# Kernel optimization log

Hardware: AMD Instinct MI355X
Metric: run time of the kernel (lower is better)

The kernel has to match this reference:

```python
import jax, jax.numpy as jnp
import numpy as np

CLUSTER_DIM = 64
SHRINKAGE = True
EPS = 1e-8


def setup_inputs() -> dict:
    key = jax.random.key(0)
    x = jax.random.normal(key, (256, CLUSTER_DIM, 4096), dtype=jnp.float32)
    return {"x": x}


def _mat_shrinkage(C, n):
    # Rao-Blackwellized Ledoit-Wolf shrinkage toward scaled identity.
    p = CLUSTER_DIM
    I = jnp.eye(p, dtype=C.dtype)[None, :, :]
    trace = jnp.trace(C, axis1=-2, axis2=-1)[:, None, None]          # [B,1,1]
    F_hat = trace / p * I
    second_trace = jnp.einsum('bij,bji->b', C, C)[:, None, None]      # tr(C @ C)
    numerator = (n - 2) / n * second_trace + trace ** 2
    denominator = (n + 2) * (second_trace - trace ** 2 / p)
    rho = jnp.minimum(numerator / denominator, 1.0)
    return rho * F_hat + (1.0 - rho) * C


def reference(x):
    B, C, M = x.shape  # C == CLUSTER_DIM
    x_mu = jnp.mean(x, axis=2, keepdims=True)
    x_cnt = x - x_mu                                                  # [B,C,M]
    cov = jnp.einsum('bcm,bdm->bcd', x_cnt, x_cnt) / M                # [B,C,C]
    if SHRINKAGE:
        cov = _mat_shrinkage(cov, n=M)
    L, Q = jnp.linalg.eigh(cov)                                       # L:[B,C] Q:[B,C,C]
    L = jnp.maximum(L, EPS)
    # S_hat = Q @ diag(L^-1/2) @ Q^T, fused as scaled columns of Q
    S_hat = jnp.einsum('bik,bk,bjk->bij', Q, jax.lax.rsqrt(L), Q)     # [B,C,C]
    Z = jnp.einsum('bij,bjm->bim', S_hat, x_cnt)                      # [B,C,M]
    return Z
```

## Files before the change

kernel.cpp:

```cpp
#include <hip/hip_runtime.h>
#include <hip/hip_bf16.h>

#define BB 256
#define P 64
#define MM 4096
#define MC 128
#define MT 256

using bf16x8 = __attribute__((ext_vector_type(8))) short;
using f32x16 = __attribute__((ext_vector_type(16))) float;

__device__ inline unsigned bfh(float a) {
    unsigned u = __float_as_uint(a);
    return (u + 0x7fffu + ((u >> 16) & 1u)) >> 16;
}
__device__ inline f32x16 MF(bf16x8 a, bf16x8 b, f32x16 c) {
    return __builtin_amdgcn_mfma_f32_32x32x16_bf16(a, b, c, 0, 0, 0);
}

__global__ __launch_bounds__(256)
void covpart_kernel(const float* __restrict__ x, float* __restrict__ s2p,
                    float* __restrict__ s1p, int nsplit)
{
    __shared__ __align__(16) unsigned char smem[17408];
    char* xh = (char*)smem;

    const int b = blockIdx.x, sp = blockIdx.y;
    const int t = threadIdx.x;
    const int w = t >> 6, l = t & 63;
    const int lr = l & 31, lh = l >> 5;
    const int mlen = MM / nsplit;
    const float* xb = x + (size_t)b * (P * MM) + (size_t)sp * mlen;

    f32x16 acc0 = {0,0,0,0,0,0,0,0,0,0,0,0,0,0,0,0};
    f32x16 acc1 = {0,0,0,0,0,0,0,0,0,0,0,0,0,0,0,0};
    f32x16 acc2 = {0,0,0,0,0,0,0,0,0,0,0,0,0,0,0,0};
    float s1a[8] = {0.f,0.f,0.f,0.f,0.f,0.f,0.f,0.f};

    const int kbase = lh * 16;

    const int nch = mlen / MC;
    for (int ch = 0; ch < nch; ++ch) {
        const int m0 = ch * MC;
        __syncthreads();
        float4 v[8];
        #pragma unroll
        for (int j = 0; j < 8; ++j) {
            int f4 = t + 256 * j;
            int r = f4 >> 5, c = (f4 & 31) << 2;
            v[j] = *reinterpret_cast<const float4*>(xb + (size_t)r * MM + m0 + c);
        }
        #pragma unroll
        for (int j = 0; j < 8; ++j) {
            int f4 = t + 256 * j;
            int r = f4 >> 5, c4 = f4 & 31;
            float e0 = v[j].x, e1 = v[j].y, e2 = v[j].z, e3 = v[j].w;
            s1a[j] += (e0 + e1) + (e2 + e3);
            uint2 hp;
            hp.x = bfh(e0) | (bfh(e1) << 16);
            hp.y = bfh(e2) | (bfh(e3) << 16);
            *reinterpret_cast<uint2*>(xh + r * 272 + c4 * 8) = hp;
        }
        __syncthreads();
        #pragma unroll
        for (int kk = 0; kk < 2; ++kk) {
            const int kb = (2 * w + kk) * 32 + kbase;
            bf16x8 f0 = *(const bf16x8*)(xh + lr * 272 + kb);
            bf16x8 f1 = *(const bf16x8*)(xh + (32 + lr) * 272 + kb);
            acc0 = MF(f0, f0, acc0);
            acc1 = MF(f0, f1, acc1);
            acc2 = MF(f1, f1, acc2);
        }
    }

    float (*T)[32][33] = reinterpret_cast<float (*)[32][33]>(smem);
    float* s2b = s2p + ((size_t)sp * BB + b) * (P * P);

#define REDUCE_PASS(ACC, STORE)                                       \
    {                                                                 \
        __syncthreads();                                              \
        _Pragma("unroll")                                             \
        for (int n = 0; n < 16; ++n) {                                \
            int row = (n & 3) + 8 * (n >> 2) + 4 * lh;                \
            T[w][row][lr] = ACC[n];                                   \
        }                                                             \
        __syncthreads();                                              \
        _Pragma("unroll")                                             \
        for (int q = 0; q < 4; ++q) {                                 \
            int idx = t + 256 * q;                                    \
            int r = idx >> 5, c = idx & 31;                           \
            float s = T[0][r][c] + T[1][r][c] + T[2][r][c] + T[3][r][c]; \
            STORE                                                     \
        }                                                             \
    }

    REDUCE_PASS(acc0, s2b[r * 64 + c] = s;)
    REDUCE_PASS(acc1, s2b[r * 64 + 32 + c] = s; s2b[(32 + c) * 64 + r] = s;)
    REDUCE_PASS(acc2, s2b[(32 + r) * 64 + 32 + c] = s;)
#undef REDUCE_PASS

    #pragma unroll
    for (int m = 16; m >= 1; m >>= 1) {
        #pragma unroll
        for (int j = 0; j < 8; ++j) s1a[j] += __shfl_xor(s1a[j], m);
    }
    if ((l & 31) == 0) {
        float* s1b = s1p + ((size_t)sp * BB + b) * P;
        int r0 = 2 * w + lh;
        #pragma unroll
        for (int j = 0; j < 8; ++j) s1b[r0 + 8 * j] = s1a[j];
    }
}

typedef float (*Mat68)[68];

__device__ inline void mm64f(Mat68 D, Mat68 A, Mat68 Bm, int t, float alpha, float beta)
{
    __syncthreads();
    const int r0 = (t >> 4) * 4, c0 = (t & 15) * 4;
    float acc[4][4];
    #pragma unroll
    for (int i = 0; i < 4; ++i)
        #pragma unroll
        for (int j = 0; j < 4; ++j) acc[i][j] = 0.f;
    #pragma unroll 4
    for (int k = 0; k < P; ++k) {
        float av[4], bv[4];
        *reinterpret_cast<float4*>(av) = *reinterpret_cast<const float4*>(&A[k][r0]);
        *reinterpret_cast<float4*>(bv) = *reinterpret_cast<const float4*>(&Bm[k][c0]);
        #pragma unroll
        for (int i = 0; i < 4; ++i)
            #pragma unroll
            for (int j = 0; j < 4; ++j) acc[i][j] += av[i] * bv[j];
    }
    __syncthreads();
    #pragma unroll
    for (int i = 0; i < 4; ++i)
        #pragma unroll
        for (int j = 0; j < 4; ++j)
            D[r0 + i][c0 + j] = alpha * acc[i][j] + ((r0 + i) == (c0 + j) ? beta : 0.f);
}

__global__ __launch_bounds__(256)
void whiten_kernel(const float* __restrict__ s2p, const float* __restrict__ s1p,
                   float* __restrict__ shat, float* __restrict__ tvec, int nsplit)
{
    __shared__ __align__(16) float B0[P][68], B1[P][68], B2[P][68], B3[P][68], B4[P][68];
    __shared__ float mus[P];
    __shared__ float red[2][4];
    const int b = blockIdx.x, t = threadIdx.x;

    if (t < P) {
        float s = 0.f;
        for (int sp = 0; sp < nsplit; ++sp) s += s1p[((size_t)sp * BB + b) * P + t];
        mus[t] = s * (1.0f / MM);
    }
    __syncthreads();

    float tr_part = 0.f, s2_part = 0.f;
    #pragma unroll
    for (int j = 0; j < 16; ++j) {
        int f = t + 256 * j;
        int i = f >> 6, jc = f & 63;
        float sum = 0.f;
        for (int sp = 0; sp < nsplit; ++sp)
            sum += s2p[((size_t)sp * BB + b) * (P * P) + f];
        float v = sum * (1.0f / MM) - mus[i] * mus[jc];
        B0[i][jc] = v;
        s2_part += v * v;
        if (i == jc) tr_part += v;
    }
    #pragma unroll
    for (int off = 32; off > 0; off >>= 1) {
        tr_part += __shfl_down(tr_part, off);
        s2_part += __shfl_down(s2_part, off);
    }
    if ((t & 63) == 0) { red[0][t >> 6] = tr_part; red[1][t >> 6] = s2_part; }
    __syncthreads();
    const float trace = red[0][0] + red[0][1] + red[0][2] + red[0][3];
    const float sum2  = red[1][0] + red[1][1] + red[1][2] + red[1][3];

    const float nf = (float)MM;
    const float num = (nf - 2.0f) / nf * sum2 + trace * trace;
    const float den = (nf + 2.0f) * (sum2 - trace * trace / (float)P);
    const float rho = (den > 0.f) ? fminf(num / den, 1.0f) : 1.0f;
    const float lam = trace * (1.0f / P);
    const float inv_s = 1.0f / lam;

    #pragma unroll
    for (int j = 0; j < 16; ++j) {
        int f = t + 256 * j;
        int i = f >> 6, jc = f & 63;
        float v = B0[i][jc];
        float sv = ((1.0f - rho) * v + ((i == jc) ? rho * lam : 0.f)) * inv_s;
        B0[i][jc] = sv;
        B2[i][jc] = ((i == jc) ? 1.5f : 0.f) - 0.5f * sv;
    }

    mm64f(B1, B0, B2, t, 1.f, 0.f);
    Mat68 Yc = B1, Zc = B2, Tc = B0, U = B3, V = B4;
    {
        mm64f(Tc, Zc, Yc, t, -0.5f, 1.5f);
        mm64f(U,  Yc, Tc, t, 1.f, 0.f);
        mm64f(V,  Tc, Zc, t, 1.f, 0.f);
        Mat68 tmp = Yc; Yc = U; U = tmp;
        tmp = Zc; Zc = V; V = tmp;
    }
    mm64f(Tc, Zc, Yc, t, -0.5f, 1.5f);
    mm64f(U,  Tc, Zc, t, 1.f, 0.f);
    __syncthreads();

    const float sc = rsqrtf(lam);
    float* sb = shat + (size_t)b * (P * P);
    #pragma unroll
    for (int j = 0; j < 16; ++j) {
        int f = t + 256 * j;
        int i = f >> 6, jc = f & 63;
        sb[f] = U[i][jc] * sc;
    }
    if (t < P) {
        float tv = 0.f;
        #pragma unroll
        for (int d = 0; d < P; ++d) tv += U[t][d] * mus[d];
        tvec[b * P + t] = tv * sc;
    }
}

__global__ __launch_bounds__(256)
void apply_kernel(const float* __restrict__ x, const float* __restrict__ shat,
                  const float* __restrict__ tvec, float* __restrict__ out)
{
    __shared__ __align__(16) float Ss[P][P];
    __shared__ __align__(16) float Xs[P][MT];
    const int mt = blockIdx.x, b = blockIdx.y;
    const int t = threadIdx.x;
    const float* xb = x + (size_t)b * (P * MM) + mt * MT;
    const float* sb = shat + (size_t)b * (P * P);

    #pragma unroll
    for (int j = 0; j < 4; ++j) {
        int f4 = t + 256 * j;
        *reinterpret_cast<float4*>(&Ss[f4 >> 4][(f4 & 15) * 4]) =
            *reinterpret_cast<const float4*>(sb + (size_t)f4 * 4);
    }
    #pragma unroll
    for (int j = 0; j < 16; ++j) {
        int f4 = t + 256 * j;
        int r = f4 >> 6, c = (f4 & 63) * 4;
        *reinterpret_cast<float4*>(&Xs[r][c]) =
            *reinterpret_cast<const float4*>(xb + (size_t)r * MM + c);
    }
    __syncthreads();

    const int w = t >> 6, l = t & 63;
    const int r0 = (w & 1) * 32 + (l >> 4) * 8;
    const int c0 = (w >> 1) * 128 + (l & 15) * 4;
    float acc[8][8];
    #pragma unroll
    for (int i = 0; i < 8; ++i)
        #pragma unroll
        for (int j = 0; j < 8; ++j) acc[i][j] = 0.f;

    for (int d = 0; d < P; ++d) {
        float sv[8], xv[8];
        *reinterpret_cast<float4*>(&sv[0]) = *reinterpret_cast<const float4*>(&Ss[d][r0]);
        *reinterpret_cast<float4*>(&sv[4]) = *reinterpret_cast<const float4*>(&Ss[d][r0 + 4]);
        *reinterpret_cast<float4*>(&xv[0]) = *reinterpret_cast<const float4*>(&Xs[d][c0]);
        *reinterpret_cast<float4*>(&xv[4]) = *reinterpret_cast<const float4*>(&Xs[d][c0 + 64]);
        #pragma unroll
        for (int i = 0; i < 8; ++i)
            #pragma unroll
            for (int j = 0; j < 8; ++j)
                acc[i][j] += sv[i] * xv[j];
    }

    float tv[8];
    *reinterpret_cast<float4*>(&tv[0]) = *reinterpret_cast<const float4*>(tvec + b * P + r0);
    *reinterpret_cast<float4*>(&tv[4]) = *reinterpret_cast<const float4*>(tvec + b * P + r0 + 4);
    float* ob = out + (size_t)b * (P * MM) + mt * MT;
    #pragma unroll
    for (int i = 0; i < 8; ++i) {
        float4 v0 = make_float4(acc[i][0] - tv[i], acc[i][1] - tv[i],
                                acc[i][2] - tv[i], acc[i][3] - tv[i]);
        float4 v1 = make_float4(acc[i][4] - tv[i], acc[i][5] - tv[i],
                                acc[i][6] - tv[i], acc[i][7] - tv[i]);
        *reinterpret_cast<float4*>(ob + (size_t)(r0 + i) * MM + c0)      = v0;
        *reinterpret_cast<float4*>(ob + (size_t)(r0 + i) * MM + c0 + 64) = v1;
    }
}

extern "C" void kernel_launch(void* const* d_in, const int* in_sizes, int n_in,
                              void* d_out, int out_size, void* d_ws, size_t ws_size,
                              hipStream_t stream)
{
    const float* x = (const float*)d_in[0];
    float* out = (float*)d_out;

    auto need = [](int ns) -> size_t {
        return ((size_t)ns * BB * P * P + (size_t)ns * BB * P
                + (size_t)BB * P * P + (size_t)BB * P) * sizeof(float);
    };
    int nsplit = 4;
    if (ws_size < need(4)) nsplit = 2;
    if (ws_size < need(2)) nsplit = 1;

    float* s2p  = (float*)d_ws;
    float* s1p  = s2p + (size_t)nsplit * BB * P * P;
    float* shat = s1p + (size_t)nsplit * BB * P;
    float* tvec = shat + (size_t)BB * P * P;

    covpart_kernel<<<dim3(BB, nsplit), 256, 0, stream>>>(x, s2p, s1p, nsplit);
    whiten_kernel<<<dim3(BB), 256, 0, stream>>>(s2p, s1p, shat, tvec, nsplit);
    apply_kernel<<<dim3(MM / MT, BB), 256, 0, stream>>>(x, shat, tvec, out);
}
```

Measured before the change: 215.8 us.

## Use bf16 MFMA for the whitening apply GEMM and hardware bf16 pack

The apply kernel now stages the whitening matrix as bf16 and packs pairs of x rows into bf16 in shared memory, then computes the 64x256 output tile with 32x32x16 bf16 MFMA instead of an fp32 FMA outer-product loop. The whiten kernel writes the scaled whitening matrix directly as packed bf16. The software round-to-nearest bf16 conversion in the covariance kernel is replaced by the v_cvt_pk_bf16_f32 instruction. This removes most of the scalar FMA work in the apply stage at the cost of bf16 precision on the output GEMM and scalar, less coalesced output stores.

```diff
diff --git a/kernel.cpp b/kernel.cpp
--- a/kernel.cpp
+++ b/kernel.cpp
@@ -10,12 +10,13 @@
 using bf16x8 = __attribute__((ext_vector_type(8))) short;
 using f32x16 = __attribute__((ext_vector_type(16))) float;
 
-__device__ inline unsigned bfh(float a) {
-    unsigned u = __float_as_uint(a);
-    return (u + 0x7fffu + ((u >> 16) & 1u)) >> 16;
-}
 __device__ inline f32x16 MF(bf16x8 a, bf16x8 b, f32x16 c) {
     return __builtin_amdgcn_mfma_f32_32x32x16_bf16(a, b, c, 0, 0, 0);
+}
+__device__ inline unsigned cvtpk(float lo, float hi) {
+    unsigned u;
+    asm("v_cvt_pk_bf16_f32 %0, %1, %2" : "=v"(u) : "v"(lo), "v"(hi));
+    return u;
 }
 
 __global__ __launch_bounds__(256)
@@ -57,8 +58,8 @@
             float e0 = v[j].x, e1 = v[j].y, e2 = v[j].z, e3 = v[j].w;
             s1a[j] += (e0 + e1) + (e2 + e3);
             uint2 hp;
-            hp.x = bfh(e0) | (bfh(e1) << 16);
-            hp.y = bfh(e2) | (bfh(e3) << 16);
+            hp.x = cvtpk(e0, e1);
+            hp.y = cvtpk(e2, e3);
             *reinterpret_cast<uint2*>(xh + r * 272 + c4 * 8) = hp;
         }
         __syncthreads();
@@ -143,7 +144,7 @@
 
 __global__ __launch_bounds__(256)
 void whiten_kernel(const float* __restrict__ s2p, const float* __restrict__ s1p,
-                   float* __restrict__ shat, float* __restrict__ tvec, int nsplit)
+                   unsigned* __restrict__ sbb, float* __restrict__ tvec, int nsplit)
 {
     __shared__ __align__(16) float B0[P][68], B1[P][68], B2[P][68], B3[P][68], B4[P][68];
     __shared__ float mus[P];
@@ -211,12 +212,12 @@
     __syncthreads();
 
     const float sc = rsqrtf(lam);
-    float* sb = shat + (size_t)b * (P * P);
-    #pragma unroll
-    for (int j = 0; j < 16; ++j) {
-        int f = t + 256 * j;
-        int i = f >> 6, jc = f & 63;
-        sb[f] = U[i][jc] * sc;
+    unsigned* sb = sbb + (size_t)b * (P * P / 2);
+    #pragma unroll
+    for (int j = 0; j < 8; ++j) {
+        int f2 = t + 256 * j;
+        int i = f2 >> 5, jc = (f2 & 31) * 2;
+        sb[f2] = cvtpk(U[i][jc] * sc, U[i][jc + 1] * sc);
     }
     if (t < P) {
         float tv = 0.f;
@@ -227,66 +228,79 @@
 }
 
 __global__ __launch_bounds__(256)
-void apply_kernel(const float* __restrict__ x, const float* __restrict__ shat,
+void apply_kernel(const float* __restrict__ x, const unsigned* __restrict__ sbb,
                   const float* __restrict__ tvec, float* __restrict__ out)
 {
-    __shared__ __align__(16) float Ss[P][P];
-    __shared__ __align__(16) float Xs[P][MT];
+    __shared__ __align__(16) unsigned short Sb[P][72];
+    __shared__ __align__(16) unsigned Xpk[32][260];
+    __shared__ float tvs[P];
     const int mt = blockIdx.x, b = blockIdx.y;
     const int t = threadIdx.x;
+    const int w = t >> 6, l = t & 63;
+    const int lr = l & 31, lh = l >> 5;
+
+    const unsigned* sb = sbb + (size_t)b * (P * P / 2);
+    #pragma unroll
+    for (int j = 0; j < 8; ++j) {
+        int slot = t + 256 * j;
+        int row = slot >> 5, cu = slot & 31;
+        *reinterpret_cast<unsigned*>(&Sb[row][cu * 2]) = sb[slot];
+    }
+    if (t < P) tvs[t] = tvec[b * P + t];
+
     const float* xb = x + (size_t)b * (P * MM) + mt * MT;
-    const float* sb = shat + (size_t)b * (P * P);
-
-    #pragma unroll
-    for (int j = 0; j < 4; ++j) {
-        int f4 = t + 256 * j;
-        *reinterpret_cast<float4*>(&Ss[f4 >> 4][(f4 & 15) * 4]) =
-            *reinterpret_cast<const float4*>(sb + (size_t)f4 * 4);
-    }
-    #pragma unroll
-    for (int j = 0; j < 16; ++j) {
-        int f4 = t + 256 * j;
-        int r = f4 >> 6, c = (f4 & 63) * 4;
-        *reinterpret_cast<float4*>(&Xs[r][c]) =
-            *reinterpret_cast<const float4*>(xb + (size_t)r * MM + c);
-    }
-    __syncthreads();
-
-    const int w = t >> 6, l = t & 63;
-    const int r0 = (w & 1) * 32 + (l >> 4) * 8;
-    const int c0 = (w >> 1) * 128 + (l & 15) * 4;
-    float acc[8][8];
-    #pragma unroll
-    for (int i = 0; i < 8; ++i)
-        #pragma unroll
-        for (int j = 0; j < 8; ++j) acc[i][j] = 0.f;
-
-    for (int d = 0; d < P; ++d) {
-        float sv[8], xv[8];
-        *reinterpret_cast<float4*>(&sv[0]) = *reinterpret_cast<const float4*>(&Ss[d][r0]);
-        *reinterpret_cast<float4*>(&sv[4]) = *reinterpret_cast<const float4*>(&Ss[d][r0 + 4]);
-        *reinterpret_cast<float4*>(&xv[0]) = *reinterpret_cast<const float4*>(&Xs[d][c0]);
-        *reinterpret_cast<float4*>(&xv[4]) = *reinterpret_cast<const float4*>(&Xs[d][c0 + 64]);
-        #pragma unroll
-        for (int i = 0; i < 8; ++i)
-            #pragma unroll
-            for (int j = 0; j < 8; ++j)
-                acc[i][j] += sv[i] * xv[j];
-    }
-
-    float tv[8];
-    *reinterpret_cast<float4*>(&tv[0]) = *reinterpret_cast<const float4*>(tvec + b * P + r0);
-    *reinterpret_cast<float4*>(&tv[4]) = *reinterpret_cast<const float4*>(tvec + b * P + r0 + 4);
+    #pragma unroll
+    for (int j = 0; j < 8; ++j) {
+        int slot = t + 256 * j;
+        int dp = slot >> 6, m0 = (slot & 63) * 4;
+        const float* xr = xb + (size_t)(2 * dp) * MM + m0;
+        float4 a = *reinterpret_cast<const float4*>(xr);
+        float4 c = *reinterpret_cast<const float4*>(xr + MM);
+        unsigned u0 = cvtpk(a.x, c.x), u1 = cvtpk(a.y, c.y);
+        unsigned u2 = cvtpk(a.z, c.z), u3 = cvtpk(a.w, c.w);
+        uint4 pk = make_uint4(u0, u1, u2, u3);
+        *reinterpret_cast<uint4*>(&Xpk[dp][m0]) = pk;
+    }
+    __syncthreads();
+
+    f32x16 acc00 = {0,0,0,0,0,0,0,0,0,0,0,0,0,0,0,0};
+    f32x16 acc01 = {0,0,0,0,0,0,0,0,0,0,0,0,0,0,0,0};
+    f32x16 acc10 = {0,0,0,0,0,0,0,0,0,0,0,0,0,0,0,0};
+    f32x16 acc11 = {0,0,0,0,0,0,0,0,0,0,0,0,0,0,0,0};
+
+    const int cq0 = (2 * w) * 32 + lr, cq1 = (2 * w + 1) * 32 + lr;
+    #pragma unroll
+    for (int ks = 0; ks < 4; ++ks) {
+        const char* arow = (const char*)&Sb[0][0] + ks * 32 + lh * 16;
+        bf16x8 a0 = *(const bf16x8*)(arow + lr * 144);
+        bf16x8 a1 = *(const bf16x8*)(arow + (32 + lr) * 144);
+        const int dpb = ks * 8 + lh * 4;
+        union { unsigned u[4]; bf16x8 v; } b0, b1;
+        #pragma unroll
+        for (int q = 0; q < 4; ++q) {
+            b0.u[q] = Xpk[dpb + q][cq0];
+            b1.u[q] = Xpk[dpb + q][cq1];
+        }
+        acc00 = MF(a0, b0.v, acc00);
+        acc01 = MF(a0, b1.v, acc01);
+        acc10 = MF(a1, b0.v, acc10);
+        acc11 = MF(a1, b1.v, acc11);
+    }
+
     float* ob = out + (size_t)b * (P * MM) + mt * MT;
-    #pragma unroll
-    for (int i = 0; i < 8; ++i) {
-        float4 v0 = make_float4(acc[i][0] - tv[i], acc[i][1] - tv[i],
-                                acc[i][2] - tv[i], acc[i][3] - tv[i]);
-        float4 v1 = make_float4(acc[i][4] - tv[i], acc[i][5] - tv[i],
-                                acc[i][6] - tv[i], acc[i][7] - tv[i]);
-        *reinterpret_cast<float4*>(ob + (size_t)(r0 + i) * MM + c0)      = v0;
-        *reinterpret_cast<float4*>(ob + (size_t)(r0 + i) * MM + c0 + 64) = v1;
-    }
+#define STORE_TILE(ACC, RT, CQ)                                          \
+    {                                                                    \
+        _Pragma("unroll")                                                \
+        for (int n = 0; n < 16; ++n) {                                   \
+            int row = (RT) * 32 + (n & 3) + 8 * (n >> 2) + 4 * lh;       \
+            ob[(size_t)row * MM + (CQ)] = ACC[n] - tvs[row];             \
+        }                                                                \
+    }
+    STORE_TILE(acc00, 0, cq0)
+    STORE_TILE(acc01, 0, cq1)
+    STORE_TILE(acc10, 1, cq0)
+    STORE_TILE(acc11, 1, cq1)
+#undef STORE_TILE
 }
 
 extern "C" void kernel_launch(void* const* d_in, const int* in_sizes, int n_in,
@@ -298,7 +312,7 @@
 
     auto need = [](int ns) -> size_t {
         return ((size_t)ns * BB * P * P + (size_t)ns * BB * P
-                + (size_t)BB * P * P + (size_t)BB * P) * sizeof(float);
+                + (size_t)BB * P * P / 2 + (size_t)BB * P) * sizeof(float);
     };
     int nsplit = 4;
     if (ws_size < need(4)) nsplit = 2;
@@ -306,10 +320,10 @@
 
     float* s2p  = (float*)d_ws;
     float* s1p  = s2p + (size_t)nsplit * BB * P * P;
-    float* shat = s1p + (size_t)nsplit * BB * P;
-    float* tvec = shat + (size_t)BB * P * P;
+    unsigned* sbb = (unsigned*)(s1p + (size_t)nsplit * BB * P);
+    float* tvec = (float*)(sbb + (size_t)BB * P * P / 2);
 
     covpart_kernel<<<dim3(BB, nsplit), 256, 0, stream>>>(x, s2p, s1p, nsplit);
-    whiten_kernel<<<dim3(BB), 256, 0, stream>>>(s2p, s1p, shat, tvec, nsplit);
-    apply_kernel<<<dim3(MM / MT, BB), 256, 0, stream>>>(x, shat, tvec, out);
-}
+    whiten_kernel<<<dim3(BB), 256, 0, stream>>>(s2p, s1p, sbb, tvec, nsplit);
+    apply_kernel<<<dim3(MM / MT, BB), 256, 0, stream>>>(x, sbb, tvec, out);
+}
```

Result: faster. 196.2 us (-9.1%).
